# Kernel tuning notes

Measured on AMD Instinct MI355X. Metric: run time of the kernel, lower is better.

The kernel has to match this reference:

```python
import jax, jax.numpy as jnp
import numpy as np

B, D, C = 2048, 1024, 8192


def setup_inputs() -> dict:
    key = jax.random.key(0)
    k1, k2, k3 = jax.random.split(key, 3)
    x = jax.random.normal(k1, (B, D), dtype=jnp.float32)
    y = jax.random.randint(k2, (B,), 0, C)
    centroids = jax.random.normal(k3, (C, D), dtype=jnp.float32)
    return {"x": x, "y": y, "centroids": centroids}


def reference(x, y, centroids):
    x2 = jnp.sum(x * x, axis=-1, keepdims=True)          # (B, 1)
    c2 = jnp.sum(centroids * centroids, axis=-1)          # (C,)
    logits = -(x2 + c2[None, :] - 2.0 * (x @ centroids.T))  # (B, C)
    decisions = jnp.argmax(logits, axis=1)                # nearest centroid
    score = jnp.mean((decisions == y).astype(jnp.float32))
    # CrossEntropyLoss(distances, y)
    logp = jax.nn.log_softmax(logits, axis=-1)
    loss = -jnp.mean(jnp.take_along_axis(logp, y[:, None], axis=1))
    return loss, score
```

## Files before the change

kernel.cpp:

```cpp
#include <hip/hip_runtime.h>
#include <cstdint>

#define MDIM 2048
#define KDIM 1024
#define CDIM 8192
#define BM 128
#define BN 128
#define BK 32
#define NCHUNK (2 * (CDIM / BN))

typedef __attribute__((ext_vector_type(8))) __bf16 bf16x8;
typedef __attribute__((ext_vector_type(4))) float f32x4;

__device__ __forceinline__ unsigned short f2bf(float f) {
  unsigned u = __float_as_uint(f);
  u += 0x7fffu + ((u >> 16) & 1u);
  return (unsigned short)(u >> 16);
}

__device__ __forceinline__ void async_ld16(const void* g, void* l) {
  __builtin_amdgcn_global_load_lds(
      (__attribute__((address_space(1))) void*)(g),
      (__attribute__((address_space(3))) void*)(l),
      16, 0, 0);
}

__global__ __launch_bounds__(256) void convert_all(const float* __restrict__ x,
                                                   const float* __restrict__ cent,
                                                   unsigned short* __restrict__ xb,
                                                   unsigned short* __restrict__ cb,
                                                   float* __restrict__ c2) {
  const int b = blockIdx.x, t = threadIdx.x;
  if (b < MDIM) {
    const float4 v = ((const float4*)(x + (size_t)b * KDIM))[t];
    ushort4 o;
    o.x = f2bf(v.x); o.y = f2bf(v.y); o.z = f2bf(v.z); o.w = f2bf(v.w);
    ((ushort4*)(xb + (size_t)b * KDIM))[t] = o;
  } else {
    const int row = b - MDIM;
    const float4 v = ((const float4*)(cent + (size_t)row * KDIM))[t];
    ushort4 o;
    o.x = f2bf(v.x); o.y = f2bf(v.y); o.z = f2bf(v.z); o.w = f2bf(v.w);
    ((ushort4*)(cb + (size_t)row * KDIM))[t] = o;
    float p = v.x * v.x + v.y * v.y + v.z * v.z + v.w * v.w;
    for (int d = 32; d; d >>= 1) p += __shfl_down(p, d, 64);
    __shared__ float red[4];
    if ((t & 63) == 0) red[t >> 6] = p;
    __syncthreads();
    if (t == 0) c2[row] = red[0] + red[1] + red[2] + red[3];
  }
}

__global__ __launch_bounds__(256) void gemm_reduce(
    const unsigned short* __restrict__ Ab, const unsigned short* __restrict__ Bb,
    const float* __restrict__ c2,
    float* __restrict__ pm, float* __restrict__ pl, int* __restrict__ pidx) {
  __shared__ __align__(16) unsigned short As[BM * BK];
  __shared__ __align__(16) unsigned short Bs[BN * BK];
  const int tid = threadIdx.x;
  const int wave = tid >> 6, lane = tid & 63;
  const int wm = wave >> 1, wn = wave & 1;
  const int bn = blockIdx.x, bm = blockIdx.y;
  const int quad = lane >> 4, c16 = lane & 15;

  f32x4 acc[4][4] = {};

  const int srow = lane >> 2;
  const int scol = (lane & 3) * 8;
  const unsigned short* ag = Ab + (size_t)(bm * BM + wave * 32 + srow) * KDIM + scol;
  const unsigned short* bg = Bb + (size_t)(bn * BN + wave * 32 + srow) * KDIM + scol;
  unsigned short* asl = &As[(wave * 32) * BK];
  unsigned short* bsl = &Bs[(wave * 32) * BK];

  for (int k0 = 0; k0 < KDIM; k0 += BK) {
    async_ld16(ag + k0, asl);
    async_ld16(ag + k0 + 16 * KDIM, asl + 16 * BK);
    async_ld16(bg + k0, bsl);
    async_ld16(bg + k0 + 16 * KDIM, bsl + 16 * BK);
    __syncthreads();
    bf16x8 a[4], b[4];
#pragma unroll
    for (int mt = 0; mt < 4; ++mt)
      a[mt] = *(const bf16x8*)&As[(wm * 64 + mt * 16 + c16) * BK + quad * 8];
#pragma unroll
    for (int nt = 0; nt < 4; ++nt)
      b[nt] = *(const bf16x8*)&Bs[(wn * 64 + nt * 16 + c16) * BK + quad * 8];
#pragma unroll
    for (int mt = 0; mt < 4; ++mt)
#pragma unroll
      for (int nt = 0; nt < 4; ++nt)
        acc[mt][nt] = __builtin_amdgcn_mfma_f32_16x16x32_bf16(a[mt], b[nt], acc[mt][nt], 0, 0, 0);
    __syncthreads();
  }

  const int colbase = bn * BN + wn * 64;
  float c2v[4];
#pragma unroll
  for (int nt = 0; nt < 4; ++nt) c2v[nt] = c2[colbase + nt * 16 + c16];

  const int chunk = bn * 2 + wn;
#pragma unroll
  for (int mt = 0; mt < 4; ++mt) {
#pragma unroll
    for (int r = 0; r < 4; ++r) {
      float sv[4];
#pragma unroll
      for (int nt = 0; nt < 4; ++nt) sv[nt] = 2.0f * acc[mt][nt][r] - c2v[nt];
      float m = sv[0];
      int idx = colbase + c16;
#pragma unroll
      for (int nt = 1; nt < 4; ++nt) {
        if (sv[nt] > m) { m = sv[nt]; idx = colbase + nt * 16 + c16; }
      }
      float l = 0.f;
#pragma unroll
      for (int nt = 0; nt < 4; ++nt) l += __expf(sv[nt] - m);
      for (int d = 1; d < 16; d <<= 1) {
        float om = __shfl_xor(m, d, 64);
        float ol = __shfl_xor(l, d, 64);
        int oi = __shfl_xor(idx, d, 64);
        float M = fmaxf(m, om);
        l = l * __expf(m - M) + ol * __expf(om - M);
        idx = (om > m || (om == m && oi < idx)) ? oi : idx;
        m = M;
      }
      if (c16 == 0) {
        const int row = bm * BM + wm * 64 + mt * 16 + quad * 4 + r;
        pm[(size_t)row * NCHUNK + chunk] = m;
        pl[(size_t)row * NCHUNK + chunk] = l;
        pidx[(size_t)row * NCHUNK + chunk] = idx;
      }
    }
  }
}

__global__ __launch_bounds__(128) void combine_kernel(
    const float* __restrict__ pm, const float* __restrict__ pl,
    const int* __restrict__ pidx, const float* __restrict__ x,
    const float* __restrict__ cent, const float* __restrict__ c2,
    const int* __restrict__ y,
    float* __restrict__ loss_part, float* __restrict__ corr_part) {
  const int row = blockIdx.x, t = threadIdx.x;
  const int yc = y[row];

  float m = pm[(size_t)row * NCHUNK + t];
  float l = pl[(size_t)row * NCHUNK + t];
  int idx = pidx[(size_t)row * NCHUNK + t];

  const float4* xa = (const float4*)(x + (size_t)row * KDIM) + t * 2;
  const float4* ca = (const float4*)(cent + (size_t)yc * KDIM) + t * 2;
  const float4 a0 = xa[0], a1 = xa[1], b0 = ca[0], b1 = ca[1];
  float dot = a0.x * b0.x + a0.y * b0.y + a0.z * b0.z + a0.w * b0.w
            + a1.x * b1.x + a1.y * b1.y + a1.z * b1.z + a1.w * b1.w;

  for (int d = 1; d < 64; d <<= 1) {
    const float om = __shfl_xor(m, d, 64);
    const float ol = __shfl_xor(l, d, 64);
    const int oi = __shfl_xor(idx, d, 64);
    const float od = __shfl_xor(dot, d, 64);
    const float M = fmaxf(m, om);
    l = l * __expf(m - M) + ol * __expf(om - M);
    idx = (om > m || (om == m && oi < idx)) ? oi : idx;
    m = M;
    dot += od;
  }
  __shared__ float sm[2], sl[2], sd[2];
  __shared__ int si[2];
  if ((t & 63) == 0) { sm[t >> 6] = m; sl[t >> 6] = l; si[t >> 6] = idx; sd[t >> 6] = dot; }
  __syncthreads();
  if (t == 0) {
    const float m0 = sm[0], m1 = sm[1];
    const float M = fmaxf(m0, m1);
    const float L = sl[0] * __expf(m0 - M) + sl[1] * __expf(m1 - M);
    int g;
    if (m1 > m0 || (m1 == m0 && si[1] < si[0])) g = si[1]; else g = si[0];
    const float sy = 2.0f * (sd[0] + sd[1]) - c2[yc];
    loss_part[row] = __logf(L) + M - sy;
    corr_part[row] = (g == yc) ? 1.f : 0.f;
  }
}

__global__ __launch_bounds__(256) void finalize(const float* __restrict__ loss_part,
                                                const float* __restrict__ corr_part,
                                                float* __restrict__ out) {
  const int t = threadIdx.x;
  float s0 = 0.f, s1 = 0.f;
  for (int i = t; i < MDIM; i += 256) { s0 += loss_part[i]; s1 += corr_part[i]; }
  for (int d = 32; d; d >>= 1) {
    s0 += __shfl_down(s0, d, 64);
    s1 += __shfl_down(s1, d, 64);
  }
  __shared__ float r0[4], r1[4];
  if ((t & 63) == 0) { r0[t >> 6] = s0; r1[t >> 6] = s1; }
  __syncthreads();
  if (t == 0) {
    out[0] = (r0[0] + r0[1] + r0[2] + r0[3]) * (1.0f / MDIM);
    out[1] = (r1[0] + r1[1] + r1[2] + r1[3]) * (1.0f / MDIM);
  }
}

extern "C" void kernel_launch(void* const* d_in, const int* in_sizes, int n_in,
                              void* d_out, int out_size, void* d_ws, size_t ws_size,
                              hipStream_t stream) {
  const float* x = (const float*)d_in[0];
  const int* y = (const int*)d_in[1];
  const float* cent = (const float*)d_in[2];
  float* out = (float*)d_out;

  char* ws = (char*)d_ws;
  const size_t OFF_XB = 0;
  const size_t OFF_CB = OFF_XB + (size_t)MDIM * KDIM * 2;
  const size_t OFF_C2 = OFF_CB + (size_t)CDIM * KDIM * 2;
  const size_t OFF_PM = OFF_C2 + (size_t)CDIM * 4;
  const size_t OFF_PL = OFF_PM + (size_t)NCHUNK * MDIM * 4;
  const size_t OFF_PI = OFF_PL + (size_t)NCHUNK * MDIM * 4;
  const size_t OFF_LP = OFF_PI + (size_t)NCHUNK * MDIM * 4;
  const size_t OFF_CP = OFF_LP + (size_t)MDIM * 4;
  const size_t NEED = OFF_CP + (size_t)MDIM * 4;
  if (ws_size < NEED) return;

  unsigned short* xb = (unsigned short*)(ws + OFF_XB);
  unsigned short* cb = (unsigned short*)(ws + OFF_CB);
  float* c2 = (float*)(ws + OFF_C2);
  float* pm = (float*)(ws + OFF_PM);
  float* pl = (float*)(ws + OFF_PL);
  int* pidx = (int*)(ws + OFF_PI);
  float* loss_part = (float*)(ws + OFF_LP);
  float* corr_part = (float*)(ws + OFF_CP);

  convert_all<<<MDIM + CDIM, 256, 0, stream>>>(x, cent, xb, cb, c2);
  gemm_reduce<<<dim3(CDIM / BN, MDIM / BM), 256, 0, stream>>>(xb, cb, c2, pm, pl, pidx);
  combine_kernel<<<MDIM, 128, 0, stream>>>(pm, pl, pidx, x, cent, c2, y, loss_part, corr_part);
  finalize<<<1, 256, 0, stream>>>(loss_part, corr_part, out);
}
```

Baseline: 153.5 us.

## Fuse fp32-to-bf16 conversion into GEMM tile loads, drop pre-convert pass

```diff
diff --git a/kernel.cpp b/kernel.cpp
--- a/kernel.cpp
+++ b/kernel.cpp
@@ -12,12 +12,6 @@
 typedef __attribute__((ext_vector_type(8))) __bf16 bf16x8;
 typedef __attribute__((ext_vector_type(4))) float f32x4;
 
-__device__ __forceinline__ unsigned short f2bf(float f) {
-  unsigned u = __float_as_uint(f);
-  u += 0x7fffu + ((u >> 16) & 1u);
-  return (unsigned short)(u >> 16);
-}
-
 __device__ __forceinline__ void async_ld16(const void* g, void* l) {
   __builtin_amdgcn_global_load_lds(
       (__attribute__((address_space(1))) void*)(g),
@@ -25,38 +19,25 @@
       16, 0, 0);
 }
 
-__global__ __launch_bounds__(256) void convert_all(const float* __restrict__ x,
-                                                   const float* __restrict__ cent,
-                                                   unsigned short* __restrict__ xb,
-                                                   unsigned short* __restrict__ cb,
-                                                   float* __restrict__ c2) {
-  const int b = blockIdx.x, t = threadIdx.x;
-  if (b < MDIM) {
-    const float4 v = ((const float4*)(x + (size_t)b * KDIM))[t];
-    ushort4 o;
-    o.x = f2bf(v.x); o.y = f2bf(v.y); o.z = f2bf(v.z); o.w = f2bf(v.w);
-    ((ushort4*)(xb + (size_t)b * KDIM))[t] = o;
-  } else {
-    const int row = b - MDIM;
-    const float4 v = ((const float4*)(cent + (size_t)row * KDIM))[t];
-    ushort4 o;
-    o.x = f2bf(v.x); o.y = f2bf(v.y); o.z = f2bf(v.z); o.w = f2bf(v.w);
-    ((ushort4*)(cb + (size_t)row * KDIM))[t] = o;
-    float p = v.x * v.x + v.y * v.y + v.z * v.z + v.w * v.w;
-    for (int d = 32; d; d >>= 1) p += __shfl_down(p, d, 64);
-    __shared__ float red[4];
-    if ((t & 63) == 0) red[t >> 6] = p;
-    __syncthreads();
-    if (t == 0) c2[row] = red[0] + red[1] + red[2] + red[3];
-  }
+__global__ __launch_bounds__(256) void c2_kernel(const float* __restrict__ cent,
+                                                 float* __restrict__ c2) {
+  const int row = blockIdx.x, t = threadIdx.x;
+  const float4 v = ((const float4*)(cent + (size_t)row * KDIM))[t];
+  float p = v.x * v.x + v.y * v.y + v.z * v.z + v.w * v.w;
+  for (int d = 32; d; d >>= 1) p += __shfl_down(p, d, 64);
+  __shared__ float red[4];
+  if ((t & 63) == 0) red[t >> 6] = p;
+  __syncthreads();
+  if (t == 0) c2[row] = red[0] + red[1] + red[2] + red[3];
 }
 
 __global__ __launch_bounds__(256) void gemm_reduce(
-    const unsigned short* __restrict__ Ab, const unsigned short* __restrict__ Bb,
+    const float* __restrict__ A,
+    const float* __restrict__ Bf,
     const float* __restrict__ c2,
     float* __restrict__ pm, float* __restrict__ pl, int* __restrict__ pidx) {
-  __shared__ __align__(16) unsigned short As[BM * BK];
-  __shared__ __align__(16) unsigned short Bs[BN * BK];
+  __shared__ __align__(16) float As[BM * BK];
+  __shared__ __align__(16) float Bs[BN * BK];
   const int tid = threadIdx.x;
   const int wave = tid >> 6, lane = tid & 63;
   const int wm = wave >> 1, wn = wave & 1;
@@ -65,26 +46,42 @@
 
   f32x4 acc[4][4] = {};
 
-  const int srow = lane >> 2;
-  const int scol = (lane & 3) * 8;
-  const unsigned short* ag = Ab + (size_t)(bm * BM + wave * 32 + srow) * KDIM + scol;
-  const unsigned short* bg = Bb + (size_t)(bn * BN + wave * 32 + srow) * KDIM + scol;
-  unsigned short* asl = &As[(wave * 32) * BK];
-  unsigned short* bsl = &Bs[(wave * 32) * BK];
+  const int srow8 = lane >> 3;
+  const int sg = (lane & 7) ^ srow8;
+  const float* agb = A + (size_t)(bm * BM + wave * 32 + srow8) * KDIM + sg * 4;
+  const float* bgb = Bf + (size_t)(bn * BN + wave * 32 + srow8) * KDIM + sg * 4;
 
   for (int k0 = 0; k0 < KDIM; k0 += BK) {
-    async_ld16(ag + k0, asl);
-    async_ld16(ag + k0 + 16 * KDIM, asl + 16 * BK);
-    async_ld16(bg + k0, bsl);
-    async_ld16(bg + k0 + 16 * KDIM, bsl + 16 * BK);
+#pragma unroll
+    for (int g = 0; g < 4; ++g) {
+      async_ld16(agb + (size_t)(g * 8) * KDIM + k0, &As[(wave * 32 + g * 8) * BK]);
+      async_ld16(bgb + (size_t)(g * 8) * KDIM + k0, &Bs[(wave * 32 + g * 8) * BK]);
+    }
     __syncthreads();
+
     bf16x8 a[4], b[4];
 #pragma unroll
-    for (int mt = 0; mt < 4; ++mt)
-      a[mt] = *(const bf16x8*)&As[(wm * 64 + mt * 16 + c16) * BK + quad * 8];
-#pragma unroll
-    for (int nt = 0; nt < 4; ++nt)
-      b[nt] = *(const bf16x8*)&Bs[(wn * 64 + nt * 16 + c16) * BK + quad * 8];
+    for (int mt = 0; mt < 4; ++mt) {
+      const int r = wm * 64 + mt * 16 + c16;
+      const int s = c16 & 7;
+      const float4 f0 = *(const float4*)&As[r * BK + (((quad * 2) ^ s) * 4)];
+      const float4 f1 = *(const float4*)&As[r * BK + (((quad * 2 + 1) ^ s) * 4)];
+      a[mt][0] = (__bf16)f0.x; a[mt][1] = (__bf16)f0.y;
+      a[mt][2] = (__bf16)f0.z; a[mt][3] = (__bf16)f0.w;
+      a[mt][4] = (__bf16)f1.x; a[mt][5] = (__bf16)f1.y;
+      a[mt][6] = (__bf16)f1.z; a[mt][7] = (__bf16)f1.w;
+    }
+#pragma unroll
+    for (int nt = 0; nt < 4; ++nt) {
+      const int r = wn * 64 + nt * 16 + c16;
+      const int s = c16 & 7;
+      const float4 f0 = *(const float4*)&Bs[r * BK + (((quad * 2) ^ s) * 4)];
+      const float4 f1 = *(const float4*)&Bs[r * BK + (((quad * 2 + 1) ^ s) * 4)];
+      b[nt][0] = (__bf16)f0.x; b[nt][1] = (__bf16)f0.y;
+      b[nt][2] = (__bf16)f0.z; b[nt][3] = (__bf16)f0.w;
+      b[nt][4] = (__bf16)f1.x; b[nt][5] = (__bf16)f1.y;
+      b[nt][6] = (__bf16)f1.z; b[nt][7] = (__bf16)f1.w;
+    }
 #pragma unroll
     for (int mt = 0; mt < 4; ++mt)
 #pragma unroll
@@ -208,9 +205,7 @@
   float* out = (float*)d_out;
 
   char* ws = (char*)d_ws;
-  const size_t OFF_XB = 0;
-  const size_t OFF_CB = OFF_XB + (size_t)MDIM * KDIM * 2;
-  const size_t OFF_C2 = OFF_CB + (size_t)CDIM * KDIM * 2;
+  const size_t OFF_C2 = 0;
   const size_t OFF_PM = OFF_C2 + (size_t)CDIM * 4;
   const size_t OFF_PL = OFF_PM + (size_t)NCHUNK * MDIM * 4;
   const size_t OFF_PI = OFF_PL + (size_t)NCHUNK * MDIM * 4;
@@ -219,8 +214,6 @@
   const size_t NEED = OFF_CP + (size_t)MDIM * 4;
   if (ws_size < NEED) return;
 
-  unsigned short* xb = (unsigned short*)(ws + OFF_XB);
-  unsigned short* cb = (unsigned short*)(ws + OFF_CB);
   float* c2 = (float*)(ws + OFF_C2);
   float* pm = (float*)(ws + OFF_PM);
   float* pl = (float*)(ws + OFF_PL);
@@ -228,8 +221,8 @@
   float* loss_part = (float*)(ws + OFF_LP);
   float* corr_part = (float*)(ws + OFF_CP);
 
-  convert_all<<<MDIM + CDIM, 256, 0, stream>>>(x, cent, xb, cb, c2);
-  gemm_reduce<<<dim3(CDIM / BN, MDIM / BM), 256, 0, stream>>>(xb, cb, c2, pm, pl, pidx);
+  c2_kernel<<<CDIM, 256, 0, stream>>>(cent, c2);
+  gemm_reduce<<<dim3(CDIM / BN, MDIM / BM), 256, 0, stream>>>(x, cent, c2, pm, pl, pidx);
   combine_kernel<<<MDIM, 128, 0, stream>>>(pm, pl, pidx, x, cent, c2, y, loss_part, corr_part);
   finalize<<<1, 256, 0, stream>>>(loss_part, corr_part, out);
 }
```

Measured after the change: 174.0 us. 1.13x slower.

## Use wave-per-row prep and two-pass max-then-sum reductions in epilogue

Applied to the files above, without the earlier changes.

```diff
diff --git a/kernel.cpp b/kernel.cpp
--- a/kernel.cpp
+++ b/kernel.cpp
@@ -25,29 +25,42 @@
       16, 0, 0);
 }
 
-__global__ __launch_bounds__(256) void convert_all(const float* __restrict__ x,
-                                                   const float* __restrict__ cent,
-                                                   unsigned short* __restrict__ xb,
-                                                   unsigned short* __restrict__ cb,
-                                                   float* __restrict__ c2) {
-  const int b = blockIdx.x, t = threadIdx.x;
-  if (b < MDIM) {
-    const float4 v = ((const float4*)(x + (size_t)b * KDIM))[t];
-    ushort4 o;
-    o.x = f2bf(v.x); o.y = f2bf(v.y); o.z = f2bf(v.z); o.w = f2bf(v.w);
-    ((ushort4*)(xb + (size_t)b * KDIM))[t] = o;
+__global__ __launch_bounds__(256) void prep(const float* __restrict__ x,
+                                            const float* __restrict__ cent,
+                                            unsigned short* __restrict__ xb,
+                                            unsigned short* __restrict__ cb,
+                                            float* __restrict__ c2) {
+  const int wave = threadIdx.x >> 6, lane = threadIdx.x & 63;
+  const int row = blockIdx.x * 4 + wave;
+  if (row < MDIM) {
+    const float4* src = (const float4*)(x + (size_t)row * KDIM);
+    ushort4* dst = (ushort4*)(xb + (size_t)row * KDIM);
+    float4 v[4];
+#pragma unroll
+    for (int i = 0; i < 4; ++i) v[i] = src[lane + 64 * i];
+#pragma unroll
+    for (int i = 0; i < 4; ++i) {
+      ushort4 o;
+      o.x = f2bf(v[i].x); o.y = f2bf(v[i].y); o.z = f2bf(v[i].z); o.w = f2bf(v[i].w);
+      dst[lane + 64 * i] = o;
+    }
   } else {
-    const int row = b - MDIM;
-    const float4 v = ((const float4*)(cent + (size_t)row * KDIM))[t];
-    ushort4 o;
-    o.x = f2bf(v.x); o.y = f2bf(v.y); o.z = f2bf(v.z); o.w = f2bf(v.w);
-    ((ushort4*)(cb + (size_t)row * KDIM))[t] = o;
-    float p = v.x * v.x + v.y * v.y + v.z * v.z + v.w * v.w;
+    const int r = row - MDIM;
+    const float4* src = (const float4*)(cent + (size_t)r * KDIM);
+    ushort4* dst = (ushort4*)(cb + (size_t)r * KDIM);
+    float4 v[4];
+#pragma unroll
+    for (int i = 0; i < 4; ++i) v[i] = src[lane + 64 * i];
+    float p = 0.f;
+#pragma unroll
+    for (int i = 0; i < 4; ++i) {
+      ushort4 o;
+      o.x = f2bf(v[i].x); o.y = f2bf(v[i].y); o.z = f2bf(v[i].z); o.w = f2bf(v[i].w);
+      dst[lane + 64 * i] = o;
+      p += v[i].x * v[i].x + v[i].y * v[i].y + v[i].z * v[i].z + v[i].w * v[i].w;
+    }
     for (int d = 32; d; d >>= 1) p += __shfl_down(p, d, 64);
-    __shared__ float red[4];
-    if ((t & 63) == 0) red[t >> 6] = p;
-    __syncthreads();
-    if (t == 0) c2[row] = red[0] + red[1] + red[2] + red[3];
+    if (lane == 0) c2[r] = p;
   }
 }
 
@@ -112,18 +125,13 @@
       for (int nt = 1; nt < 4; ++nt) {
         if (sv[nt] > m) { m = sv[nt]; idx = colbase + nt * 16 + c16; }
       }
-      float l = 0.f;
-#pragma unroll
-      for (int nt = 0; nt < 4; ++nt) l += __expf(sv[nt] - m);
       for (int d = 1; d < 16; d <<= 1) {
-        float om = __shfl_xor(m, d, 64);
-        float ol = __shfl_xor(l, d, 64);
-        int oi = __shfl_xor(idx, d, 64);
-        float M = fmaxf(m, om);
-        l = l * __expf(m - M) + ol * __expf(om - M);
-        idx = (om > m || (om == m && oi < idx)) ? oi : idx;
-        m = M;
+        const float om = __shfl_xor(m, d, 64);
+        const int oi = __shfl_xor(idx, d, 64);
+        if (om > m || (om == m && oi < idx)) { m = om; idx = oi; }
       }
+      float l = __expf(sv[0] - m) + __expf(sv[1] - m) + __expf(sv[2] - m) + __expf(sv[3] - m);
+      for (int d = 1; d < 16; d <<= 1) l += __shfl_xor(l, d, 64);
       if (c16 == 0) {
         const int row = bm * BM + wm * 64 + mt * 16 + quad * 4 + r;
         pm[(size_t)row * NCHUNK + chunk] = m;
@@ -153,29 +161,31 @@
   float dot = a0.x * b0.x + a0.y * b0.y + a0.z * b0.z + a0.w * b0.w
             + a1.x * b1.x + a1.y * b1.y + a1.z * b1.z + a1.w * b1.w;
 
+  float M = m;
+  int gidx = idx;
   for (int d = 1; d < 64; d <<= 1) {
-    const float om = __shfl_xor(m, d, 64);
-    const float ol = __shfl_xor(l, d, 64);
-    const int oi = __shfl_xor(idx, d, 64);
+    const float om = __shfl_xor(M, d, 64);
+    const int oi = __shfl_xor(gidx, d, 64);
     const float od = __shfl_xor(dot, d, 64);
-    const float M = fmaxf(m, om);
-    l = l * __expf(m - M) + ol * __expf(om - M);
-    idx = (om > m || (om == m && oi < idx)) ? oi : idx;
-    m = M;
+    if (om > M || (om == M && oi < gidx)) { M = om; gidx = oi; }
     dot += od;
   }
-  __shared__ float sm[2], sl[2], sd[2];
+  __shared__ float sm[2], sd[2];
   __shared__ int si[2];
-  if ((t & 63) == 0) { sm[t >> 6] = m; sl[t >> 6] = l; si[t >> 6] = idx; sd[t >> 6] = dot; }
+  if ((t & 63) == 0) { sm[t >> 6] = M; si[t >> 6] = gidx; sd[t >> 6] = dot; }
+  __syncthreads();
+  const float Mg = fmaxf(sm[0], sm[1]);
+  float lr = l * __expf(m - Mg);
+  for (int d = 1; d < 64; d <<= 1) lr += __shfl_xor(lr, d, 64);
+  __shared__ float sl[2];
+  if ((t & 63) == 0) sl[t >> 6] = lr;
   __syncthreads();
   if (t == 0) {
-    const float m0 = sm[0], m1 = sm[1];
-    const float M = fmaxf(m0, m1);
-    const float L = sl[0] * __expf(m0 - M) + sl[1] * __expf(m1 - M);
+    const float L = sl[0] + sl[1];
     int g;
-    if (m1 > m0 || (m1 == m0 && si[1] < si[0])) g = si[1]; else g = si[0];
+    if (sm[1] > sm[0] || (sm[1] == sm[0] && si[1] < si[0])) g = si[1]; else g = si[0];
     const float sy = 2.0f * (sd[0] + sd[1]) - c2[yc];
-    loss_part[row] = __logf(L) + M - sy;
+    loss_part[row] = __logf(L) + Mg - sy;
     corr_part[row] = (g == yc) ? 1.f : 0.f;
   }
 }
@@ -228,7 +238,7 @@
   float* loss_part = (float*)(ws + OFF_LP);
   float* corr_part = (float*)(ws + OFF_CP);
 
-  convert_all<<<MDIM + CDIM, 256, 0, stream>>>(x, cent, xb, cb, c2);
+  prep<<<(MDIM + CDIM) / 4, 256, 0, stream>>>(x, cent, xb, cb, c2);
   gemm_reduce<<<dim3(CDIM / BN, MDIM / BM), 256, 0, stream>>>(xb, cb, c2, pm, pl, pidx);
   combine_kernel<<<MDIM, 128, 0, stream>>>(pm, pl, pidx, x, cent, c2, y, loss_part, corr_part);
   finalize<<<1, 256, 0, stream>>>(loss_part, corr_part, out);
```

New measurement: 157.7 us. 1.03x slower.
